# Kernel tuning notes

Measured on AMD Instinct MI355X. Metric: run time of the kernel, lower is better.

The kernel has to match this reference:

```python
import jax, jax.numpy as jnp
import numpy as np

B, T, N, F = 16, 12, 1024, 128
H, DH, C = 8, 16, 64  # heads, d_head (=d_core//H), core_num; note d_in must equal H*DH
EPS = 1e-5


def setup_inputs() -> dict:
    key = jax.random.key(0)
    ks = jax.random.split(key, 12)
    s = lambda fan_in: 1.0 / np.sqrt(fan_in)
    return {
        "input": jax.random.normal(ks[0], (B, T, N, F), jnp.float32),
        # value Linear(d_in,d_in); weights stored [in,out]
        "W_v": jax.random.normal(ks[1], (F, F), jnp.float32) * s(F),
        "b_v": jax.random.normal(ks[2], (F,), jnp.float32) * s(F),
        # core decomposition params
        "adaptive": jax.random.normal(ks[3], (H, DH, N), jnp.float32),
        "cores": jax.random.normal(ks[4], (H, C, DH), jnp.float32),
        # FFN: Linear(2F -> 8F), GELU, Linear(8F -> F)
        "W1": jax.random.normal(ks[5], (2 * F, 8 * F), jnp.float32) * s(2 * F),
        "b1": jax.random.normal(ks[6], (8 * F,), jnp.float32) * s(2 * F),
        "W2": jax.random.normal(ks[7], (8 * F, F), jnp.float32) * s(8 * F),
        "b2": jax.random.normal(ks[8], (F,), jnp.float32) * s(8 * F),
        # BatchNorm2d(d_in) affine params (training-mode batch stats)
        "gamma": jnp.ones((F,), jnp.float32),
        "beta": jnp.zeros((F,), jnp.float32),
    }


def reference(input, W_v, b_v, adaptive, cores, W1, b1, W2, b2, gamma, beta):
    b, t, n, f = input.shape
    h, dh, _ = adaptive.shape
    # value projection, split heads: [b,t,n,f] -> [b,t,h,dh,n]
    v = input @ W_v + b_v
    v = v.reshape(b, t, n, h, dh).transpose(0, 1, 3, 4, 2)
    # core affinity scores [h,c,n]
    aff = jnp.einsum("hcd,hdn->hcn", cores, adaptive) / np.sqrt(dh)
    a_n2c = jax.nn.softmax(aff, axis=-1)  # softmax over nodes
    a_c2n = jax.nn.softmax(aff, axis=-2)  # softmax over cores
    # two-stage aggregation through cores
    v = jnp.einsum("bthfn,hcn->bthfc", v, a_n2c)
    v = jnp.einsum("bthfc,hcn->bthfn", v, a_c2n)
    # merge heads: [b,t,h,dh,n] -> [b,t,f,n] -> [b,t,n,f]
    v = v.reshape(b, t, f, n).swapaxes(-1, -2)
    # FFN on concat([input - v, v]) (dropout off in eval), residual
    x = jnp.concatenate([input - v, v], axis=-1)
    x = jax.nn.gelu(x @ W1 + b1, approximate=False) @ W2 + b2
    out = x + input
    # BatchNorm2d over channel f (batch stats over b,t,n; biased variance)
    mean = out.mean(axis=(0, 1, 2))
    var = out.var(axis=(0, 1, 2))
    return (out - mean) * jax.lax.rsqrt(var + EPS) * gamma + beta
```

## Files before the change

kernel.cpp:

```cpp
#include <hip/hip_runtime.h>
#include <math.h>

#define BB 16
#define TT 12
#define NN 1024
#define FF 128
#define BT 192
#define BTN 196608
#define CNT ((float)BTN)
#define T1SZ 1572864

typedef unsigned short ushort_t;
typedef __attribute__((ext_vector_type(8))) short bf16x8;
typedef __attribute__((ext_vector_type(4))) float f32x4;

__device__ __forceinline__ ushort_t f2bf(float x) {
    union { float f; unsigned u; } c; c.f = x;
    unsigned r = c.u + 0x7fffu + ((c.u >> 16) & 1u);
    return (ushort_t)(r >> 16);
}
__device__ __forceinline__ float bf2f(ushort_t u) {
    union { unsigned u32; float f; } c; c.u32 = ((unsigned)u) << 16; return c.f;
}
__device__ __forceinline__ unsigned pk2(float a, float b) {
    return (unsigned)f2bf(a) | ((unsigned)f2bf(b) << 16);
}
__device__ __forceinline__ float gelu_f(float x) {
    float u = x * x;
    float s = x * fmaf(u, -0.10294428f, -2.30220852f);
    float e = __builtin_amdgcn_exp2f(s);
    return x * __builtin_amdgcn_rcpf(1.0f + e);
}

__device__ __forceinline__ char* swz512(void* base, int row, int byteoff) {
    return (char*)base + row * 512 + (byteoff ^ ((row & 7) << 4));
}
__device__ __forceinline__ char* swz256(void* base, int row, int byteoff) {
    return (char*)base + row * 256 + (byteoff ^ ((row & 7) << 4));
}

__global__ __launch_bounds__(256) void k_aff(const float* __restrict__ cores,
                                             const float* __restrict__ adaptive,
                                             float* __restrict__ aff) {
    int idx = blockIdx.x * 256 + threadIdx.x;
    int n  = idx & 1023;
    int hc = idx >> 10;
    int h  = hc >> 6;
    const float* cp = cores + hc * 16;
    const float* ap = adaptive + h * 16384 + n;
    float s = 0.f;
#pragma unroll
    for (int d = 0; d < 16; ++d) s = fmaf(cp[d], ap[d * 1024], s);
    aff[idx] = s * 0.25f;
}

__global__ __launch_bounds__(256) void k_sm_n(const float* __restrict__ aff,
                                              ushort_t* __restrict__ out) {
    int row = blockIdx.x;
    const float* p = aff + row * 1024;
    int t = threadIdx.x;
    __shared__ float red[8];
    float v0 = p[t], v1 = p[t + 256], v2 = p[t + 512], v3 = p[t + 768];
    float m = fmaxf(fmaxf(v0, v1), fmaxf(v2, v3));
#pragma unroll
    for (int off = 32; off >= 1; off >>= 1) m = fmaxf(m, __shfl_xor(m, off));
    if ((t & 63) == 0) red[t >> 6] = m;
    __syncthreads();
    m = fmaxf(fmaxf(red[0], red[1]), fmaxf(red[2], red[3]));
    v0 = expf(v0 - m); v1 = expf(v1 - m); v2 = expf(v2 - m); v3 = expf(v3 - m);
    float s = v0 + v1 + v2 + v3;
#pragma unroll
    for (int off = 32; off >= 1; off >>= 1) s += __shfl_xor(s, off);
    __syncthreads();
    if ((t & 63) == 0) red[4 + (t >> 6)] = s;
    __syncthreads();
    s = red[4] + red[5] + red[6] + red[7];
    float inv = 1.0f / s;
    out[row * 1024 + t]       = f2bf(v0 * inv);
    out[row * 1024 + t + 256] = f2bf(v1 * inv);
    out[row * 1024 + t + 512] = f2bf(v2 * inv);
    out[row * 1024 + t + 768] = f2bf(v3 * inv);
}

__global__ __launch_bounds__(256) void k_sm_c(const float* __restrict__ aff,
                                              ushort_t* __restrict__ a_c2nT) {
    __shared__ ushort_t tile[64][72];
    int b = blockIdx.x;
    int h = b >> 4, n0 = (b & 15) * 64;
    int t = threadIdx.x;
    int nl = t >> 2, q = t & 3;
    const float* p = aff + h * 65536 + n0 + nl;
    float v[16];
    float m = -1e30f;
#pragma unroll
    for (int i = 0; i < 16; ++i) {
        v[i] = p[(q * 16 + i) * 1024];
        m = fmaxf(m, v[i]);
    }
    m = fmaxf(m, __shfl_xor(m, 1));
    m = fmaxf(m, __shfl_xor(m, 2));
    float s = 0.f;
#pragma unroll
    for (int i = 0; i < 16; ++i) { v[i] = expf(v[i] - m); s += v[i]; }
    s += __shfl_xor(s, 1);
    s += __shfl_xor(s, 2);
    float inv = 1.0f / s;
#pragma unroll
    for (int i = 0; i < 16; ++i) tile[nl][q * 16 + i] = f2bf(v[i] * inv);
    __syncthreads();
    ushort_t* ob = a_c2nT + ((size_t)h * 1024 + n0) * 64;
    for (int i = t; i < 512; i += 256) {
        int r = i >> 3, cq = i & 7;
        *(bf16x8*)&ob[r * 64 + cq * 8] = *(bf16x8*)&tile[r][cq * 8];
    }
}

__global__ __launch_bounds__(256) void k_wprep_v(const float* __restrict__ Wv,
                                                 ushort_t* __restrict__ WvT) {
    __shared__ float tile[64][65];
    int b = blockIdx.x;
    int r0 = (b >> 1) * 64, c0 = (b & 1) * 64;
    int t = threadIdx.x;
    for (int i = t; i < 4096; i += 256) {
        int r = i >> 6, c = i & 63;
        tile[r][c] = Wv[(size_t)(r0 + r) * 128 + c0 + c];
    }
    __syncthreads();
    for (int i = t; i < 4096; i += 256) {
        int c = i >> 6, r = i & 63;
        WvT[(size_t)(c0 + c) * 128 + r0 + r] = f2bf(tile[r][c]);
    }
}

__global__ __launch_bounds__(256) void k_wpack1(const float* __restrict__ W1,
                                                ushort_t* __restrict__ W1f) {
    int tid = blockIdx.x * 256 + threadIdx.x;
    int lane = tid & 63, jn = (tid >> 6) & 1, kk = (tid >> 7) & 7;
    int w = (tid >> 10) & 3, ch = tid >> 12;
    int lr = lane & 15, lg = lane >> 4;
    int n = ch * 128 + w * 32 + jn * 16 + lr;
    int kb = kk * 32 + lg * 8;
    ushort_t o[8];
#pragma unroll
    for (int e = 0; e < 8; ++e) o[e] = f2bf(W1[(size_t)(kb + e) * 1024 + n]);
    *(bf16x8*)&W1f[(size_t)tid * 8] = *(bf16x8*)o;
}

__global__ __launch_bounds__(256) void k_wpack2(const float* __restrict__ W2,
                                                ushort_t* __restrict__ W2f) {
    int tid = blockIdx.x * 256 + threadIdx.x;
    int lane = tid & 63, jy = (tid >> 6) & 1, kk = (tid >> 7) & 3;
    int w = (tid >> 9) & 3, ch = tid >> 11;
    int lr = lane & 15, lg = lane >> 4;
    int f = w * 32 + jy * 16 + lr;
    int kb = ch * 128 + kk * 32 + lg * 8;
    ushort_t o[8];
#pragma unroll
    for (int e = 0; e < 8; ++e) o[e] = f2bf(W2[(size_t)(kb + e) * 128 + f]);
    *(bf16x8*)&W2f[(size_t)tid * 8] = *(bf16x8*)o;
}

__global__ __launch_bounds__(256) void k_vs1(const float* __restrict__ input,
                                             const ushort_t* __restrict__ WvT,
                                             const float* __restrict__ bv,
                                             const ushort_t* __restrict__ a_n2c,
                                             float* __restrict__ T1p) {
    __shared__ __align__(16) ushort_t as_lds[128 * 128];
    __shared__ __align__(16) ushort_t vsT[128 * 128];
    int bt = blockIdx.x;
    int part = blockIdx.y;
    int t = threadIdx.x, w = t >> 6, lane = t & 63, lr = lane & 15, lg = lane >> 4;

    f32x4 t1acc[2][4];
#pragma unroll
    for (int hl = 0; hl < 2; ++hl)
#pragma unroll
        for (int mi = 0; mi < 4; ++mi) t1acc[hl][mi] = (f32x4){0.f, 0.f, 0.f, 0.f};

    for (int c8 = part * 2; c8 < part * 2 + 2; ++c8) {
        int n0 = c8 * 128;
        __syncthreads();
        for (int j = 0; j < 16; ++j) {
            int i = j * 256 + t;
            int r = i >> 5, cq = i & 31;
            float4 f = *(const float4*)&input[((size_t)(bt * 1024 + n0 + r)) * 128 + cq * 4];
            union { uint2 d; ushort_t u[4]; } o;
            o.u[0] = f2bf(f.x); o.u[1] = f2bf(f.y); o.u[2] = f2bf(f.z); o.u[3] = f2bf(f.w);
            *(uint2*)swz256(as_lds, r, cq * 8) = o.d;
        }
        __syncthreads();
        f32x4 vacc[2][8];
#pragma unroll
        for (int mi = 0; mi < 2; ++mi)
#pragma unroll
            for (int jn = 0; jn < 8; ++jn) {
                float bb = bv[jn * 16 + lr];
                vacc[mi][jn] = (f32x4){bb, bb, bb, bb};
            }
#pragma unroll
        for (int ks = 0; ks < 4; ++ks) {
            bf16x8 a[2];
#pragma unroll
            for (int mi = 0; mi < 2; ++mi)
                a[mi] = *(const bf16x8*)swz256(as_lds, w * 32 + mi * 16 + lr, ks * 64 + lg * 16);
#pragma unroll
            for (int jn = 0; jn < 8; ++jn) {
                bf16x8 bfr = *(const bf16x8*)&WvT[(size_t)(jn * 16 + lr) * 128 + ks * 32 + lg * 8];
#pragma unroll
                for (int mi = 0; mi < 2; ++mi)
                    vacc[mi][jn] = __builtin_amdgcn_mfma_f32_16x16x32_bf16(a[mi], bfr, vacc[mi][jn], 0, 0, 0);
            }
        }
#pragma unroll
        for (int mi = 0; mi < 2; ++mi)
#pragma unroll
            for (int jn = 0; jn < 8; ++jn) {
                union { uint2 d; ushort_t u[4]; } o;
                o.u[0] = f2bf(vacc[mi][jn][0]); o.u[1] = f2bf(vacc[mi][jn][1]);
                o.u[2] = f2bf(vacc[mi][jn][2]); o.u[3] = f2bf(vacc[mi][jn][3]);
                *(uint2*)swz256(vsT, jn * 16 + lr, w * 64 + mi * 32 + lg * 8) = o.d;
            }
        __syncthreads();
#pragma unroll
        for (int hl = 0; hl < 2; ++hl) {
            int h = w * 2 + hl;
#pragma unroll
            for (int ks = 0; ks < 4; ++ks) {
                bf16x8 bfr = *(const bf16x8*)swz256(vsT, h * 16 + lr, ks * 64 + lg * 16);
#pragma unroll
                for (int mi = 0; mi < 4; ++mi) {
                    bf16x8 a = *(const bf16x8*)&a_n2c[((size_t)(h * 64 + mi * 16 + lr)) * 1024 + n0 + ks * 32 + lg * 8];
                    t1acc[hl][mi] = __builtin_amdgcn_mfma_f32_16x16x32_bf16(a, bfr, t1acc[hl][mi], 0, 0, 0);
                }
            }
        }
    }
    float* op = T1p + (size_t)part * T1SZ;
#pragma unroll
    for (int hl = 0; hl < 2; ++hl) {
        int h = w * 2 + hl;
#pragma unroll
        for (int mi = 0; mi < 4; ++mi)
            *(f32x4*)&op[(((size_t)bt * 8 + h) * 16 + lr) * 64 + mi * 16 + lg * 4] = t1acc[hl][mi];
    }
}

__global__ __launch_bounds__(256) void k_t1conv(const float* __restrict__ T1p,
                                                ushort_t* __restrict__ T1t) {
    size_t i4 = ((size_t)blockIdx.x * 256 + threadIdx.x) * 4;
    float4 s = *(const float4*)&T1p[i4];
#pragma unroll
    for (int p = 1; p < 4; ++p) {
        float4 v = *(const float4*)&T1p[(size_t)p * T1SZ + i4];
        s.x += v.x; s.y += v.y; s.z += v.z; s.w += v.w;
    }
    uint2 o;
    o.x = pk2(s.x, s.y);
    o.y = pk2(s.z, s.w);
    *(uint2*)&T1t[i4] = o;
}

__global__ __launch_bounds__(256) void k_ffn(
        const float* __restrict__ input,
        const ushort_t* __restrict__ a_c2nT,
        const ushort_t* __restrict__ T1t,
        const ushort_t* __restrict__ W1f,
        const ushort_t* __restrict__ W2f,
        const float* __restrict__ b1,
        const float* __restrict__ b2,
        float* __restrict__ out,
        float* __restrict__ bn_sum,
        float* __restrict__ bn_sq) {
    __shared__ __align__(16) ushort_t x2s[64 * 256];
    __shared__ __align__(16) ushort_t hids[64 * 128];
    int bt = blockIdx.y;
    int n0 = blockIdx.x * 64;
    int t = threadIdx.x;
    int w = t >> 6, lane = t & 63, lr = lane & 15, lg = lane >> 4;
    int R0 = w * 16;
    int rowbase = bt * 1024 + n0;

    {
        const ushort_t* tp = T1t + ((size_t)(bt * 128) + lr) * 64 + lg * 8;
        const ushort_t* ap = a_c2nT + ((size_t)(n0 + R0 + lr)) * 64 + lg * 8;
#pragma unroll
        for (int h = 0; h < 8; ++h) {
            f32x4 vacc = {0.f, 0.f, 0.f, 0.f};
#pragma unroll
            for (int kk = 0; kk < 2; ++kk) {
                bf16x8 af = *(const bf16x8*)(tp + h * 1024 + kk * 32);
                bf16x8 bf = *(const bf16x8*)(ap + (size_t)h * 65536 + kk * 32);
                vacc = __builtin_amdgcn_mfma_f32_16x16x32_bf16(af, bf, vacc, 0, 0, 0);
            }
            uint2 o;
            o.x = pk2(vacc[0], vacc[1]);
            o.y = pk2(vacc[2], vacc[3]);
            *(uint2*)swz512(x2s, R0 + lr, 256 + h * 32 + lg * 8) = o;
        }
    }
#pragma unroll
    for (int j = 0; j < 8; ++j) {
        int row = R0 + j * 2 + (lane >> 5);
        int cq = lane & 31;
        float4 f = *(const float4*)&input[((size_t)rowbase + row) * 128 + cq * 4];
        union { uint2 d; ushort_t u[4]; } vm;
        vm.d = *(uint2*)swz512(x2s, row, 256 + cq * 8);
        uint2 o;
        o.x = pk2(f.x - bf2f(vm.u[0]), f.y - bf2f(vm.u[1]));
        o.y = pk2(f.z - bf2f(vm.u[2]), f.w - bf2f(vm.u[3]));
        *(uint2*)swz512(x2s, row, cq * 8) = o;
    }
    __syncthreads();

    f32x4 yacc[4][2];
#pragma unroll
    for (int mi = 0; mi < 4; ++mi)
#pragma unroll
        for (int jy = 0; jy < 2; ++jy) {
            float bb = b2[w * 32 + jy * 16 + lr];
            yacc[mi][jy] = (f32x4){bb, bb, bb, bb};
        }

    for (int ch = 0; ch < 8; ++ch) {
        bf16x8 b2r[4][2];
        {
            const ushort_t* w2p = W2f + (((size_t)(ch * 4 + w) * 4) * 2) * 512 + lane * 8;
#pragma unroll
            for (int kk = 0; kk < 4; ++kk)
#pragma unroll
                for (int jy = 0; jy < 2; ++jy)
                    b2r[kk][jy] = *(const bf16x8*)(w2p + (kk * 2 + jy) * 512);
        }

        f32x4 hacc[2][4];
#pragma unroll
        for (int jn = 0; jn < 2; ++jn) {
            f32x4 bb = *(const f32x4*)&b1[ch * 128 + w * 32 + jn * 16 + lg * 4];
#pragma unroll
            for (int mi = 0; mi < 4; ++mi) hacc[jn][mi] = bb;
        }
        const ushort_t* w1p = W1f + ((size_t)(ch * 4 + w) * 16) * 512 + lane * 8;
#pragma unroll
        for (int kk = 0; kk < 8; ++kk) {
            bf16x8 xf[4];
#pragma unroll
            for (int mi = 0; mi < 4; ++mi)
                xf[mi] = *(const bf16x8*)swz512(x2s, mi * 16 + lr, kk * 64 + lg * 16);
#pragma unroll
            for (int jn = 0; jn < 2; ++jn) {
                bf16x8 wf = *(const bf16x8*)(w1p + (kk * 2 + jn) * 512);
#pragma unroll
                for (int mi = 0; mi < 4; ++mi)
                    hacc[jn][mi] = __builtin_amdgcn_mfma_f32_16x16x32_bf16(wf, xf[mi], hacc[jn][mi], 0, 0, 0);
            }
        }
        __syncthreads();
#pragma unroll
        for (int jn = 0; jn < 2; ++jn)
#pragma unroll
            for (int mi = 0; mi < 4; ++mi) {
                uint2 o;
                o.x = pk2(gelu_f(hacc[jn][mi][0]), gelu_f(hacc[jn][mi][1]));
                o.y = pk2(gelu_f(hacc[jn][mi][2]), gelu_f(hacc[jn][mi][3]));
                *(uint2*)swz256(hids, mi * 16 + lr, w * 64 + jn * 32 + lg * 8) = o;
            }
        __syncthreads();
#pragma unroll
        for (int kk = 0; kk < 4; ++kk) {
            bf16x8 a4[4];
#pragma unroll
            for (int mi = 0; mi < 4; ++mi)
                a4[mi] = *(const bf16x8*)swz256(hids, mi * 16 + lr, kk * 64 + lg * 16);
#pragma unroll
            for (int jy = 0; jy < 2; ++jy)
#pragma unroll
                for (int mi = 0; mi < 4; ++mi)
                    yacc[mi][jy] = __builtin_amdgcn_mfma_f32_16x16x32_bf16(a4[mi], b2r[kk][jy], yacc[mi][jy], 0, 0, 0);
        }
    }

    float sacc[2] = {0.f, 0.f}, qacc[2] = {0.f, 0.f};
#pragma unroll
    for (int mi = 0; mi < 4; ++mi)
#pragma unroll
        for (int jy = 0; jy < 2; ++jy)
#pragma unroll
            for (int r = 0; r < 4; ++r) {
                int gr = rowbase + mi * 16 + lg * 4 + r;
                int gc = w * 32 + jy * 16 + lr;
                float val = yacc[mi][jy][r] + input[(size_t)gr * 128 + gc];
                out[(size_t)gr * 128 + gc] = val;
                sacc[jy] += val;
                qacc[jy] += val * val;
            }
#pragma unroll
    for (int jy = 0; jy < 2; ++jy) {
        float s = sacc[jy], q = qacc[jy];
        s += __shfl_xor(s, 16); s += __shfl_xor(s, 32);
        q += __shfl_xor(q, 16); q += __shfl_xor(q, 32);
        if (lg == 0) {
            atomicAdd(&bn_sum[w * 32 + jy * 16 + lr], s);
            atomicAdd(&bn_sq[w * 32 + jy * 16 + lr], q);
        }
    }
}

__global__ void k_bnfin(const float* __restrict__ bn_sum, const float* __restrict__ bn_sq,
                        const float* __restrict__ gamma, const float* __restrict__ beta,
                        float* __restrict__ scale, float* __restrict__ shift) {
    int f = threadIdx.x;
    float mean = bn_sum[f] * (1.0f / CNT);
    float var  = bn_sq[f]  * (1.0f / CNT) - mean * mean;
    float sc = gamma[f] * rsqrtf(var + 1e-5f);
    scale[f] = sc;
    shift[f] = beta[f] - mean * sc;
}

__global__ __launch_bounds__(256) void k_bnapply(float* __restrict__ out,
                                                 const float* __restrict__ scale,
                                                 const float* __restrict__ shift) {
    size_t idx = (size_t)blockIdx.x * 256 + threadIdx.x;
    int c = (int)((idx * 4) & 127);
    float4 v = *(float4*)&out[idx * 4];
    float4 sc = *(const float4*)&scale[c];
    float4 sh = *(const float4*)&shift[c];
    v.x = fmaf(v.x, sc.x, sh.x);
    v.y = fmaf(v.y, sc.y, sh.y);
    v.z = fmaf(v.z, sc.z, sh.z);
    v.w = fmaf(v.w, sc.w, sh.w);
    *(float4*)&out[idx * 4] = v;
}

extern "C" void kernel_launch(void* const* d_in, const int* in_sizes, int n_in,
                              void* d_out, int out_size, void* d_ws, size_t ws_size,
                              hipStream_t stream) {
    const float* input    = (const float*)d_in[0];
    const float* Wv       = (const float*)d_in[1];
    const float* bv       = (const float*)d_in[2];
    const float* adaptive = (const float*)d_in[3];
    const float* cores    = (const float*)d_in[4];
    const float* W1       = (const float*)d_in[5];
    const float* b1       = (const float*)d_in[6];
    const float* W2       = (const float*)d_in[7];
    const float* b2       = (const float*)d_in[8];
    const float* gamma    = (const float*)d_in[9];
    const float* beta     = (const float*)d_in[10];
    float* out = (float*)d_out;
    float* ws  = (float*)d_ws;

    float*    aff    = ws;
    ushort_t* a_n2c  = (ushort_t*)(ws + 524288);
    ushort_t* a_c2nT = (ushort_t*)(ws + 786432);
    ushort_t* T1t    = (ushort_t*)(ws + 1048576);
    ushort_t* W1f    = (ushort_t*)(ws + 1835008);
    ushort_t* W2f    = (ushort_t*)(ws + 1966080);
    ushort_t* WvT    = (ushort_t*)(ws + 2031616);
    float* bn_sum    = ws + 2039808;
    float* bn_sq     = bn_sum + 128;
    float* scale     = bn_sum + 256;
    float* shift     = bn_sum + 384;
    float* T1p       = ws + 2097152;

    k_aff    <<<2048, 256, 0, stream>>>(cores, adaptive, aff);
    k_sm_n   <<<512, 256, 0, stream>>>(aff, a_n2c);
    k_sm_c   <<<128, 256, 0, stream>>>(aff, a_c2nT);
    k_wprep_v<<<4, 256, 0, stream>>>(Wv, WvT);
    k_wpack1 <<<128, 256, 0, stream>>>(W1, W1f);
    k_wpack2 <<<64, 256, 0, stream>>>(W2, W2f);
    k_vs1    <<<dim3(BT, 4), 256, 0, stream>>>(input, WvT, bv, a_n2c, T1p);
    k_t1conv <<<1536, 256, 0, stream>>>(T1p, T1t);
    hipMemsetAsync(bn_sum, 0, 256 * sizeof(float), stream);
    k_ffn    <<<dim3(16, BT), 256, 0, stream>>>(input, a_c2nT, T1t, W1f, W2f,
                                                b1, b2, out, bn_sum, bn_sq);
    k_bnfin  <<<1, 128, 0, stream>>>(bn_sum, bn_sq, gamma, beta, scale, shift);
    k_bnapply<<<(out_size / 4) / 256, 256, 0, stream>>>(out, scale, shift);
}
```

Baseline: 425.0 us.

## Store FFN LDS operands in MFMA-fragment order and fuse residual subtraction

Replaces the swizzled row-major shared-memory tiles for the FFN input and hidden activations with a layout matching the MFMA fragment order. Each lane can then read its operand with one contiguous 16-byte load indexed by lane. The input-minus-v half is now computed straight from the MFMA accumulators while they are still in registers, removing a separate pass that read v back from LDS and re-quantized it. The subtraction now uses the fp32 v rather than its bf16-rounded value, which slightly changes numerics. The new write pattern may cause bank conflicts on stores.

```diff
diff --git a/kernel.cpp b/kernel.cpp
--- a/kernel.cpp
+++ b/kernel.cpp
@@ -32,9 +32,6 @@
     return x * __builtin_amdgcn_rcpf(1.0f + e);
 }
 
-__device__ __forceinline__ char* swz512(void* base, int row, int byteoff) {
-    return (char*)base + row * 512 + (byteoff ^ ((row & 7) << 4));
-}
 __device__ __forceinline__ char* swz256(void* base, int row, int byteoff) {
     return (char*)base + row * 256 + (byteoff ^ ((row & 7) << 4));
 }
@@ -271,8 +268,8 @@
         float* __restrict__ out,
         float* __restrict__ bn_sum,
         float* __restrict__ bn_sq) {
-    __shared__ __align__(16) ushort_t x2s[64 * 256];
-    __shared__ __align__(16) ushort_t hids[64 * 128];
+    __shared__ __align__(16) ushort_t x2mb[4 * 8 * 64 * 8];
+    __shared__ __align__(16) ushort_t hmb[4 * 4 * 64 * 8];
     int bt = blockIdx.y;
     int n0 = blockIdx.x * 64;
     int t = threadIdx.x;
@@ -283,6 +280,8 @@
     {
         const ushort_t* tp = T1t + ((size_t)(bt * 128) + lr) * 64 + lg * 8;
         const ushort_t* ap = a_c2nT + ((size_t)(n0 + R0 + lr)) * 64 + lg * 8;
+        ushort_t* mb = x2mb + w * 4096;
+        int wbase = ((lg >> 1) * 16 + lr) * 8 + (lg & 1) * 4;
 #pragma unroll
         for (int h = 0; h < 8; ++h) {
             f32x4 vacc = {0.f, 0.f, 0.f, 0.f};
@@ -292,23 +291,15 @@
                 bf16x8 bf = *(const bf16x8*)(ap + (size_t)h * 65536 + kk * 32);
                 vacc = __builtin_amdgcn_mfma_f32_16x16x32_bf16(af, bf, vacc, 0, 0, 0);
             }
-            uint2 o;
-            o.x = pk2(vacc[0], vacc[1]);
-            o.y = pk2(vacc[2], vacc[3]);
-            *(uint2*)swz512(x2s, R0 + lr, 256 + h * 32 + lg * 8) = o;
-        }
-    }
-#pragma unroll
-    for (int j = 0; j < 8; ++j) {
-        int row = R0 + j * 2 + (lane >> 5);
-        int cq = lane & 31;
-        float4 f = *(const float4*)&input[((size_t)rowbase + row) * 128 + cq * 4];
-        union { uint2 d; ushort_t u[4]; } vm;
-        vm.d = *(uint2*)swz512(x2s, row, 256 + cq * 8);
-        uint2 o;
-        o.x = pk2(f.x - bf2f(vm.u[0]), f.y - bf2f(vm.u[1]));
-        o.y = pk2(f.z - bf2f(vm.u[2]), f.w - bf2f(vm.u[3]));
-        *(uint2*)swz512(x2s, row, cq * 8) = o;
+            float4 inp = *(const float4*)&input[(size_t)(rowbase + R0 + lr) * 128 + h * 16 + lg * 4];
+            uint2 lft, rgt;
+            lft.x = pk2(inp.x - vacc[0], inp.y - vacc[1]);
+            lft.y = pk2(inp.z - vacc[2], inp.w - vacc[3]);
+            rgt.x = pk2(vacc[0], vacc[1]);
+            rgt.y = pk2(vacc[2], vacc[3]);
+            *(uint2*)&mb[wbase + h * 256]         = lft;
+            *(uint2*)&mb[wbase + (h + 8) * 256]   = rgt;
+        }
     }
     __syncthreads();
 
@@ -320,6 +311,8 @@
             float bb = b2[w * 32 + jy * 16 + lr];
             yacc[mi][jy] = (f32x4){bb, bb, bb, bb};
         }
+
+    int hwbase = w * 2048 + ((lg >> 1) * 16 + lr) * 8 + (lg & 1) * 4;
 
     for (int ch = 0; ch < 8; ++ch) {
         bf16x8 b2r[4][2];
@@ -345,7 +338,7 @@
             bf16x8 xf[4];
 #pragma unroll
             for (int mi = 0; mi < 4; ++mi)
-                xf[mi] = *(const bf16x8*)swz512(x2s, mi * 16 + lr, kk * 64 + lg * 16);
+                xf[mi] = *(const bf16x8*)&x2mb[mi * 4096 + kk * 512 + lane * 8];
 #pragma unroll
             for (int jn = 0; jn < 2; ++jn) {
                 bf16x8 wf = *(const bf16x8*)(w1p + (kk * 2 + jn) * 512);
@@ -362,7 +355,7 @@
                 uint2 o;
                 o.x = pk2(gelu_f(hacc[jn][mi][0]), gelu_f(hacc[jn][mi][1]));
                 o.y = pk2(gelu_f(hacc[jn][mi][2]), gelu_f(hacc[jn][mi][3]));
-                *(uint2*)swz256(hids, mi * 16 + lr, w * 64 + jn * 32 + lg * 8) = o;
+                *(uint2*)&hmb[hwbase + jn * 256 + mi * 512] = o;
             }
         __syncthreads();
 #pragma unroll
@@ -370,7 +363,7 @@
             bf16x8 a4[4];
 #pragma unroll
             for (int mi = 0; mi < 4; ++mi)
-                a4[mi] = *(const bf16x8*)swz256(hids, mi * 16 + lr, kk * 64 + lg * 16);
+                a4[mi] = *(const bf16x8*)&hmb[kk * 2048 + mi * 512 + lane * 8];
 #pragma unroll
             for (int jy = 0; jy < 2; ++jy)
 #pragma unroll
```

After: 429.1 us. About the same (+1.0%).
